# Performance work log

Hardware: AMD Instinct MI355X
Metric: run time of the kernel (lower is better)

Reference implementation:

```python
import jax, jax.numpy as jnp
import numpy as np

B, K, SZ, D = 256, 16, 512, 8

def setup_inputs() -> dict:
    key = jax.random.key(0)
    k1, k2 = jax.random.split(key)
    x = jax.random.normal(k1, (B, SZ, D), dtype=jnp.float32)
    cluster_centers = jax.random.normal(k2, (K, SZ, D), dtype=jnp.float32)
    return {"x": x, "cluster_centers": cluster_centers}

def _dists(x, centers):
    # x: [B, sz, d]; centers: [K, sz, d]
    b, sz, d = x.shape
    k = centers.shape[0]
    # fft_sz = 2 ** int(log2(2*sz - 1) + 1)  (matches n_bits computation in normalized_cc)
    fft_sz = 2 ** int(np.log2(2 * sz - 1) + 1)
    # The module's hand-rolled dft matrix is cos(-2pi kn/N) + i sin(-2pi kn/N),
    # i.e. exactly the standard DFT of the zero-padded signal -> use jnp.fft.
    Fx = jnp.fft.fft(x, n=fft_sz, axis=1)            # [B, F, d]
    Fc = jnp.fft.fft(centers, n=fft_sz, axis=1)      # [K, F, d]
    # cc(s1, s2) = real(ifft(F1 * conj(F2))), batched over all (i, j) pairs
    prod = Fx[:, None, :, :] * jnp.conj(Fc)[None, :, :, :]   # [B, K, F, d]
    cc = jnp.real(jnp.fft.ifft(prod, axis=2))                # [B, K, F, d]
    # cc_ = cat(cc[-(sz-1):], cc[:sz])  -> length 2*sz - 1 along lag axis
    cc_cat = jnp.concatenate([cc[:, :, -(sz - 1):, :], cc[:, :, :sz, :]], axis=2)
    # norms: norm1 = Frobenius norm per sample; norm2 = arange(K) (as in forward)
    norms1 = jnp.linalg.norm(x.reshape(b, -1), axis=1)       # [B]
    norms2 = jnp.arange(k, dtype=x.dtype)                    # [K]
    denom = norms1[:, None] * norms2[None, :]                # [B, K]
    denom = jnp.where(denom < 1e-9, jnp.inf, denom)
    ncc = cc_cat.sum(axis=-1) / denom[:, :, None]            # [B, K, 2sz-1]
    return ncc.max(axis=2)                                   # [B, K]

def reference(x, cluster_centers):
    dists = _dists(x, cluster_centers)
    labels = jnp.argmin(1.0 - dists, axis=1)
    return (labels, dists)
```

## Files before the change

### kernel.cpp

```cpp
#include <hip/hip_runtime.h>
#include <math.h>


#define NB 256
#define NK 16
#define NS 512
#define ND 8

typedef __bf16 bf16x8 __attribute__((ext_vector_type(8)));
typedef float floatx4 __attribute__((ext_vector_type(4)));

__global__ void pack_kernel(const float* __restrict__ c, __bf16* __restrict__ bpk)
{
    int kc = blockIdx.x;
    int L  = threadIdx.x;
    int n = L & 15, quad = L >> 4;
    const float4* src = (const float4*)(c + ((size_t)n * NS + (size_t)(kc * 4 + quad)) * ND);
    float4 a = src[0], b = src[1];
    bf16x8 v;
    v[0] = (__bf16)a.x; v[1] = (__bf16)a.y; v[2] = (__bf16)a.z; v[3] = (__bf16)a.w;
    v[4] = (__bf16)b.x; v[5] = (__bf16)b.y; v[6] = (__bf16)b.z; v[7] = (__bf16)b.w;
    *(bf16x8*)(bpk + ((size_t)kc * 64 + L) * 8) = v;
}

__global__ __launch_bounds__(256, 4) void dists_mfma(
    const float* __restrict__ x, const __bf16* __restrict__ bpk, float* __restrict__ wsf)
{
    __shared__ __align__(16) __bf16 xq[800 * 8];
    __shared__ float wred[4][16];

    const int tid = threadIdx.x;
    const int b   = blockIdx.x;
    const int q   = blockIdx.y;
    const int m0  = q * 256;

    for (int jj = tid; jj < 800; jj += 256) {
        int j = m0 + jj;
        bf16x8 v;
        if (j >= 511 && j < 1023) {
            const float4* p = (const float4*)(x + ((size_t)b * NS + (size_t)(j - 511)) * ND);
            float4 a = p[0], bb = p[1];
            v[0] = (__bf16)a.x;  v[1] = (__bf16)a.y;  v[2] = (__bf16)a.z;  v[3] = (__bf16)a.w;
            v[4] = (__bf16)bb.x; v[5] = (__bf16)bb.y; v[6] = (__bf16)bb.z; v[7] = (__bf16)bb.w;
        } else {
            #pragma unroll
            for (int e = 0; e < 8; ++e) v[e] = (__bf16)0.0f;
        }
        *(bf16x8*)(xq + (size_t)jj * 8) = v;
    }
    __syncthreads();

    const int L    = tid & 63;
    const int w    = tid >> 6;
    const int m    = L & 15;
    const int quad = L >> 4;

    const __bf16* gb = xq + 8 * (64 * w + m + quad);
    const bf16x8* Bp = (const bf16x8*)bpk;

    bf16x8 Q[16];
    #pragma unroll
    for (int i = 0; i < 16; ++i) Q[i] = *(const bf16x8*)(gb + 8 * (4 * i));

    floatx4 acc[4] = {};

    bf16x8 bcur = Bp[L];
    for (int kc0 = 0; kc0 < 128; kc0 += 16) {
        #pragma unroll
        for (int s = 0; s < 16; ++s) {
            const int kc = kc0 + s;
            bf16x8 bnxt = Bp[(size_t)((kc + 1) & 127) * 64 + L];
            bf16x8 qn = *(const bf16x8*)(gb + 8 * (4 * kc + 64));
            acc[0] = __builtin_amdgcn_mfma_f32_16x16x32_bf16(Q[(s + 0)  & 15], bcur, acc[0], 0, 0, 0);
            acc[1] = __builtin_amdgcn_mfma_f32_16x16x32_bf16(Q[(s + 4)  & 15], bcur, acc[1], 0, 0, 0);
            acc[2] = __builtin_amdgcn_mfma_f32_16x16x32_bf16(Q[(s + 8)  & 15], bcur, acc[2], 0, 0, 0);
            acc[3] = __builtin_amdgcn_mfma_f32_16x16x32_bf16(Q[(s + 12) & 15], bcur, acc[3], 0, 0, 0);
            Q[s] = qn;
            bcur = bnxt;
        }
    }

    float vmax = -INFINITY;
    #pragma unroll
    for (int r = 0; r < 4; ++r) {
        #pragma unroll
        for (int e = 0; e < 4; ++e) {
            bool phantom = (q == 3) & (w == 3) & (r == 3) & (quad == 3) & (e == 3);
            vmax = fmaxf(vmax, phantom ? -INFINITY : acc[r][e]);
        }
    }
    vmax = fmaxf(vmax, __shfl_xor(vmax, 16));
    vmax = fmaxf(vmax, __shfl_xor(vmax, 32));
    if (quad == 0) wred[w][m] = vmax;
    __syncthreads();
    if (tid < 16) {
        float mm = fmaxf(fmaxf(wred[0][tid], wred[1][tid]),
                         fmaxf(wred[2][tid], wred[3][tid]));
        wsf[((size_t)b * 4 + q) * 16 + tid] = mm;
    }
}

__global__ void finalize(const float* __restrict__ x, const float* __restrict__ wsf,
                         float* __restrict__ out)
{
    __shared__ float redn[4];
    __shared__ float dd[16];
    const int b = blockIdx.x, tid = threadIdx.x;
    const float4* x4 = (const float4*)(x + (size_t)b * (NS * ND));
    float ss = 0.f;
    #pragma unroll
    for (int i = 0; i < 4; ++i) {
        float4 v = x4[tid + 256 * i];
        ss += v.x * v.x + v.y * v.y + v.z * v.z + v.w * v.w;
    }
    #pragma unroll
    for (int off = 32; off; off >>= 1) ss += __shfl_down(ss, off);
    if ((tid & 63) == 0) redn[tid >> 6] = ss;
    __syncthreads();
    float nrm = sqrtf(redn[0] + redn[1] + redn[2] + redn[3]);
    if (tid < 16) {
        const float* wp = wsf + (size_t)b * 64 + tid;
        float mm = fmaxf(fmaxf(wp[0], wp[16]), fmaxf(wp[32], wp[48]));
        float denom = nrm * (float)tid;
        float d = (denom < 1e-9f) ? 0.f : mm / denom;
        dd[tid] = d;
        out[NB + b * NK + tid] = d;
    }
    __syncthreads();
    if (tid == 0) {
        float best = dd[0]; int lab = 0;
        #pragma unroll
        for (int k = 1; k < NK; ++k) if (dd[k] > best) { best = dd[k]; lab = k; }
        out[b] = (float)lab;
    }
}

extern "C" void kernel_launch(void* const* d_in, const int* in_sizes, int n_in,
                              void* d_out, int out_size, void* d_ws, size_t ws_size,
                              hipStream_t stream) {
    const float* x = (const float*)d_in[0];
    const float* c = (const float*)d_in[1];
    float* out = (float*)d_out;
    float* wsf = (float*)d_ws;
    __bf16* bpk = (__bf16*)((char*)d_ws + 65536);

    pack_kernel<<<128, 64, 0, stream>>>(c, bpk);
    dists_mfma<<<dim3(NB, 4), 256, 0, stream>>>(x, bpk, wsf);
    finalize<<<NB, 256, 0, stream>>>(x, wsf, out);
}
```

Baseline: 79.48 us.

## Double per-wave output tile and deepen B-operand prefetch in MFMA correlation kernel

Each block now covers 512 lag positions instead of 256, so each wave computes 8 MFMA accumulator tiles per B fragment instead of 4 and the grid shrinks from 4 to 2 blocks per sample. Each center fragment is loaded once and reused across twice as many tiles, which halves global B traffic and the redundant shared-memory staging per lag. The B prefetch becomes a 4-deep register ring instead of single-buffered. The cost is much higher register pressure (32 Q fragments plus 8 accumulators), with launch bounds lowered to 2 blocks per CU, and half as many blocks to hide latency.

```diff
diff --git a/kernel.cpp b/kernel.cpp
--- a/kernel.cpp
+++ b/kernel.cpp
@@ -6,6 +6,7 @@
 #define NK 16
 #define NS 512
 #define ND 8
+#define BAND 1040
 
 typedef __bf16 bf16x8 __attribute__((ext_vector_type(8)));
 typedef float floatx4 __attribute__((ext_vector_type(4)));
@@ -23,18 +24,18 @@
     *(bf16x8*)(bpk + ((size_t)kc * 64 + L) * 8) = v;
 }
 
-__global__ __launch_bounds__(256, 4) void dists_mfma(
+__global__ __launch_bounds__(256, 2) void dists_mfma(
     const float* __restrict__ x, const __bf16* __restrict__ bpk, float* __restrict__ wsf)
 {
-    __shared__ __align__(16) __bf16 xq[800 * 8];
+    __shared__ __align__(16) __bf16 xq[BAND * 8];
     __shared__ float wred[4][16];
 
     const int tid = threadIdx.x;
     const int b   = blockIdx.x;
-    const int q   = blockIdx.y;
-    const int m0  = q * 256;
+    const int h   = blockIdx.y;
+    const int m0  = h * 512;
 
-    for (int jj = tid; jj < 800; jj += 256) {
+    for (int jj = tid; jj < BAND; jj += 256) {
         int j = m0 + jj;
         bf16x8 v;
         if (j >= 511 && j < 1023) {
@@ -55,37 +56,43 @@
     const int m    = L & 15;
     const int quad = L >> 4;
 
-    const __bf16* gb = xq + 8 * (64 * w + m + quad);
+    const __bf16* gb = xq + 8 * (128 * w + m + quad);
     const bf16x8* Bp = (const bf16x8*)bpk;
 
-    bf16x8 Q[16];
+    bf16x8 Q[32];
     #pragma unroll
-    for (int i = 0; i < 16; ++i) Q[i] = *(const bf16x8*)(gb + 8 * (4 * i));
+    for (int i = 0; i < 32; ++i) Q[i] = *(const bf16x8*)(gb + 32 * i);
 
-    floatx4 acc[4] = {};
+    bf16x8 Bv[4];
+    #pragma unroll
+    for (int i = 0; i < 4; ++i) Bv[i] = Bp[(size_t)i * 64 + L];
 
-    bf16x8 bcur = Bp[L];
-    for (int kc0 = 0; kc0 < 128; kc0 += 16) {
+    floatx4 acc[8] = {};
+
+    for (int kc0 = 0; kc0 < 128; kc0 += 32) {
         #pragma unroll
-        for (int s = 0; s < 16; ++s) {
+        for (int s = 0; s < 32; ++s) {
             const int kc = kc0 + s;
-            bf16x8 bnxt = Bp[(size_t)((kc + 1) & 127) * 64 + L];
-            bf16x8 qn = *(const bf16x8*)(gb + 8 * (4 * kc + 64));
-            acc[0] = __builtin_amdgcn_mfma_f32_16x16x32_bf16(Q[(s + 0)  & 15], bcur, acc[0], 0, 0, 0);
-            acc[1] = __builtin_amdgcn_mfma_f32_16x16x32_bf16(Q[(s + 4)  & 15], bcur, acc[1], 0, 0, 0);
-            acc[2] = __builtin_amdgcn_mfma_f32_16x16x32_bf16(Q[(s + 8)  & 15], bcur, acc[2], 0, 0, 0);
-            acc[3] = __builtin_amdgcn_mfma_f32_16x16x32_bf16(Q[(s + 12) & 15], bcur, acc[3], 0, 0, 0);
-            Q[s] = qn;
-            bcur = bnxt;
+            bf16x8 bcur = Bv[s & 3];
+            acc[0] = __builtin_amdgcn_mfma_f32_16x16x32_bf16(Q[(s + 0)  & 31], bcur, acc[0], 0, 0, 0);
+            acc[1] = __builtin_amdgcn_mfma_f32_16x16x32_bf16(Q[(s + 4)  & 31], bcur, acc[1], 0, 0, 0);
+            acc[2] = __builtin_amdgcn_mfma_f32_16x16x32_bf16(Q[(s + 8)  & 31], bcur, acc[2], 0, 0, 0);
+            acc[3] = __builtin_amdgcn_mfma_f32_16x16x32_bf16(Q[(s + 12) & 31], bcur, acc[3], 0, 0, 0);
+            acc[4] = __builtin_amdgcn_mfma_f32_16x16x32_bf16(Q[(s + 16) & 31], bcur, acc[4], 0, 0, 0);
+            acc[5] = __builtin_amdgcn_mfma_f32_16x16x32_bf16(Q[(s + 20) & 31], bcur, acc[5], 0, 0, 0);
+            acc[6] = __builtin_amdgcn_mfma_f32_16x16x32_bf16(Q[(s + 24) & 31], bcur, acc[6], 0, 0, 0);
+            acc[7] = __builtin_amdgcn_mfma_f32_16x16x32_bf16(Q[(s + 28) & 31], bcur, acc[7], 0, 0, 0);
+            Q[s & 31] = *(const bf16x8*)(gb + 8 * (4 * kc + 128));
+            Bv[s & 3] = Bp[(size_t)((kc + 4) & 127) * 64 + L];
         }
     }
 
     float vmax = -INFINITY;
     #pragma unroll
-    for (int r = 0; r < 4; ++r) {
+    for (int r = 0; r < 8; ++r) {
         #pragma unroll
         for (int e = 0; e < 4; ++e) {
-            bool phantom = (q == 3) & (w == 3) & (r == 3) & (quad == 3) & (e == 3);
+            bool phantom = (h == 1) & (w == 3) & (r == 7) & (quad == 3) & (e == 3);
             vmax = fmaxf(vmax, phantom ? -INFINITY : acc[r][e]);
         }
     }
@@ -96,7 +103,7 @@
     if (tid < 16) {
         float mm = fmaxf(fmaxf(wred[0][tid], wred[1][tid]),
                          fmaxf(wred[2][tid], wred[3][tid]));
-        wsf[((size_t)b * 4 + q) * 16 + tid] = mm;
+        wsf[((size_t)b * 2 + h) * 16 + tid] = mm;
     }
 }
 
@@ -119,8 +126,7 @@
     __syncthreads();
     float nrm = sqrtf(redn[0] + redn[1] + redn[2] + redn[3]);
     if (tid < 16) {
-        const float* wp = wsf + (size_t)b * 64 + tid;
-        float mm = fmaxf(fmaxf(wp[0], wp[16]), fmaxf(wp[32], wp[48]));
+        float mm = fmaxf(wsf[(size_t)b * 32 + tid], wsf[(size_t)b * 32 + 16 + tid]);
         float denom = nrm * (float)tid;
         float d = (denom < 1e-9f) ? 0.f : mm / denom;
         dd[tid] = d;
@@ -145,6 +151,6 @@
     __bf16* bpk = (__bf16*)((char*)d_ws + 65536);
 
     pack_kernel<<<128, 64, 0, stream>>>(c, bpk);
-    dists_mfma<<<dim3(NB, 4), 256, 0, stream>>>(x, bpk, wsf);
+    dists_mfma<<<dim3(NB, 2), 256, 0, stream>>>(x, bpk, wsf);
     finalize<<<NB, 256, 0, stream>>>(x, wsf, out);
 }
```

Result: slower. 83.51 us (+5.1%).
